# Kernel tuning notes

Measured on AMD Instinct MI355X. Metric: run time of the kernel, lower is better.

Reference implementation:

```python
import jax, jax.numpy as jnp
import numpy as np

H = 16
EPS = 1e-5

def _layernorm(x, gamma, beta):
    mu = jnp.mean(x, axis=-1, keepdims=True)
    var = jnp.var(x, axis=-1, keepdims=True)
    return (x - mu) * jax.lax.rsqrt(var + EPS) * gamma + beta

def setup_inputs() -> dict:
    key = jax.random.key(0)
    ks = jax.random.split(key, 5)
    B, T, E = 4, 2048, 1024
    D = E // H
    return {
        "x": jax.random.normal(ks[0], (B, T, E), dtype=jnp.float32),
        "Wqkv": jax.random.normal(ks[1], (E, 3 * E), dtype=jnp.float32) * (E ** -0.5),
        "bqkv": jax.random.normal(ks[2], (3 * E,), dtype=jnp.float32) * 0.02,
        "q_gamma": jnp.ones((D,), jnp.float32),
        "q_beta": jnp.zeros((D,), jnp.float32),
        "k_gamma": jnp.ones((D,), jnp.float32),
        "k_beta": jnp.zeros((D,), jnp.float32),
        "Wproj": jax.random.normal(ks[3], (E, E), dtype=jnp.float32) * (E ** -0.5),
        "bproj": jnp.zeros((E,), jnp.float32),
    }

def reference(x, Wqkv, bqkv, q_gamma, q_beta, k_gamma, k_beta, Wproj, bproj):
    B, T, E = x.shape
    D = E // H
    qkv = x @ Wqkv + bqkv                      # [B,T,3E]
    q, k, v = jnp.split(qkv, 3, axis=-1)
    # b t (h d) -> b h t d
    to_heads = lambda a: a.reshape(B, T, H, D).transpose(0, 2, 1, 3)
    q, k, v = to_heads(q), to_heads(k), to_heads(v)
    q = _layernorm(q, q_gamma, q_beta)
    k = _layernorm(k, k_gamma, k_beta)
    scale = 1.0 / jnp.sqrt(jnp.float32(D))
    scores = jnp.einsum('bhtd,bhsd->bhts', q, k) * scale   # [B,H,T,T]
    attn = jax.nn.softmax(scores, axis=-1)
    y = jnp.einsum('bhts,bhsd->bhtd', attn, v)             # [B,H,T,D]
    y = y.transpose(0, 2, 1, 3).reshape(B, T, E)           # b h t d -> b t (h d)
    return y @ Wproj + bproj
```

## Files before the change

### kernel.cpp

```cpp
#include <hip/hip_runtime.h>

#define Hn  16
#define Dh  64
#define Bb  4
#define Tn  2048
#define En  1024
#define Mn  8192
#define N1  3072
#define Kn  1024
#define BHT (Bb*Hn*Tn)

typedef __attribute__((ext_vector_type(8)))  short  short8;
typedef __attribute__((ext_vector_type(4)))  short  short4v;
typedef __attribute__((ext_vector_type(4)))  float  f32x4;
typedef __attribute__((ext_vector_type(8)))  __bf16 bf16x8;

__device__ __forceinline__ float b2f(short s) {
  unsigned u = ((unsigned)(unsigned short)s) << 16;
  return __builtin_bit_cast(float, u);
}
__device__ __forceinline__ short f2b(float f) {
  unsigned u = __builtin_bit_cast(unsigned, f);
  u += 0x7fffu + ((u >> 16) & 1u);
  return (short)(u >> 16);
}
__device__ __forceinline__ f32x4 mfma16(short8 a, short8 b, f32x4 c) {
  return __builtin_amdgcn_mfma_f32_16x16x32_bf16(
      __builtin_bit_cast(bf16x8, a), __builtin_bit_cast(bf16x8, b), c, 0, 0, 0);
}
__device__ __forceinline__ void gload16(const void* g, void* l) {
  __builtin_amdgcn_global_load_lds(
      (const __attribute__((address_space(1))) unsigned int*)g,
      (__attribute__((address_space(3))) unsigned int*)l, 16, 0, 0);
}

__global__ __launch_bounds__(256) void cvt_x_kernel(const float* __restrict__ x,
                                                    short* __restrict__ xb) {
  const size_t i = ((size_t)blockIdx.x * 256 + threadIdx.x) * 8;
  f32x4 a = *(const f32x4*)&x[i];
  f32x4 b = *(const f32x4*)&x[i + 4];
  short8 o;
  o[0]=f2b(a[0]); o[1]=f2b(a[1]); o[2]=f2b(a[2]); o[3]=f2b(a[3]);
  o[4]=f2b(b[0]); o[5]=f2b(b[1]); o[6]=f2b(b[2]); o[7]=f2b(b[3]);
  *(short8*)&xb[i] = o;
}

__global__ __launch_bounds__(256) void transpose_w_kernel(const float* __restrict__ in,
                                                          short* __restrict__ out,
                                                          int R, int C) {
  __shared__ float tile[32][33];
  const int tid = threadIdx.x;
  const int c0 = blockIdx.x * 32, r0 = blockIdx.y * 32;
  const int lr = tid >> 3, lc = (tid & 7) * 4;
  f32x4 v = *(const f32x4*)&in[(size_t)(r0 + lr) * C + c0 + lc];
  tile[lr][lc] = v[0]; tile[lr][lc+1] = v[1]; tile[lr][lc+2] = v[2]; tile[lr][lc+3] = v[3];
  __syncthreads();
  const int oc = tid >> 3, orr = (tid & 7) * 4;
  short4v ov;
  ov[0] = f2b(tile[orr][oc]);   ov[1] = f2b(tile[orr+1][oc]);
  ov[2] = f2b(tile[orr+2][oc]); ov[3] = f2b(tile[orr+3][oc]);
  *(short4v*)&out[(size_t)(c0 + oc) * R + r0 + orr] = ov;
}

template<int MODE>
__global__ __launch_bounds__(256) void gemm_kernel(
    const short* __restrict__ A, const short* __restrict__ Bt,
    const float* __restrict__ bias, float* __restrict__ Cf,
    short* __restrict__ qo, short* __restrict__ ko2, short* __restrict__ vo,
    int N, int NBX, int cpx) {
  __shared__ short As[4096];
  __shared__ short Bs[4096];
  const int lin = blockIdx.x;
  const int swz = (lin & 7) * cpx + (lin >> 3);
  const int bx = swz % NBX, by = swz / NBX;
  const int tid = threadIdx.x, lane = tid & 63, w = tid >> 6;
  const int rowBase = by * 128, colBase = bx * 128;
  f32x4 acc[4][4] = {};
  const int srow = tid >> 2, sk = (tid & 3) << 3;
  const short* Ag = A  + (size_t)(rowBase + srow) * Kn + sk;
  const short* Bg = Bt + (size_t)(colBase + srow) * Kn + sk;
  short* AsW = As + w * 512;
  short* BsW = Bs + w * 512;
  const int ar = (w >> 1) * 64, bc = (w & 1) * 64;
  const int lg8 = (lane >> 4) * 8, lr = lane & 15;

  for (int kt = 0; kt < Kn; kt += 32) {
    __syncthreads();
    gload16(Ag + kt,            AsW);
    gload16(Ag + kt + 64 * Kn,  AsW + 2048);
    gload16(Bg + kt,            BsW);
    gload16(Bg + kt + 64 * Kn,  BsW + 2048);
    __syncthreads();
    short8 af[4], bfr[4];
#pragma unroll
    for (int m = 0; m < 4; ++m) af[m]  = *(const short8*)&As[(ar + m*16 + lr)*32 + lg8];
#pragma unroll
    for (int n = 0; n < 4; ++n) bfr[n] = *(const short8*)&Bs[(bc + n*16 + lr)*32 + lg8];
#pragma unroll
    for (int m = 0; m < 4; ++m)
#pragma unroll
      for (int n = 0; n < 4; ++n)
        acc[m][n] = mfma16(af[m], bfr[n], acc[m][n]);
  }

  const int gr0 = rowBase + ar + (lane >> 4) * 4;
  const int gc0 = colBase + bc + lr;
#pragma unroll
  for (int m = 0; m < 4; ++m) {
#pragma unroll
    for (int n = 0; n < 4; ++n) {
      const int gc = gc0 + n * 16;
      const float bb = bias[gc];
#pragma unroll
      for (int r = 0; r < 4; ++r) {
        const int gr = gr0 + m * 16 + r;
        const float v = acc[m][n][r] + bb;
        if (MODE == 0) {
          Cf[(size_t)gr * N + gc] = v;
        } else {
          const int which = gc >> 10, e = gc & 1023;
          const int hh = e >> 6, d = e & 63;
          const int bidx = gr >> 11, t = gr & 2047;
          const size_t idx = ((size_t)(bidx * Hn + hh) * Tn + t) * Dh + d;
          short* dst = (which == 0) ? qo : (which == 1) ? ko2 : vo;
          dst[idx] = f2b(v);
        }
      }
    }
  }
}

__global__ __launch_bounds__(256) void ln_qk_kernel(short* __restrict__ qp, short* __restrict__ kp,
                                                    const float* __restrict__ qg, const float* __restrict__ qb,
                                                    const float* __restrict__ kg, const float* __restrict__ kb) {
  const int lane = threadIdx.x & 63;
  const int rp = blockIdx.x * 4 + (threadIdx.x >> 6);
  const size_t base = (size_t)rp * 64 + lane;
  float xq = b2f(qp[base]);
  float xk = b2f(kp[base]);
  float sq = xq, sk = xk;
#pragma unroll
  for (int off = 1; off < 64; off <<= 1) { sq += __shfl_xor(sq, off); sk += __shfl_xor(sk, off); }
  const float muq = sq * (1.f/64), muk = sk * (1.f/64);
  const float dq = xq - muq, dk = xk - muk;
  float vq = dq * dq, vk = dk * dk;
#pragma unroll
  for (int off = 1; off < 64; off <<= 1) { vq += __shfl_xor(vq, off); vk += __shfl_xor(vk, off); }
  const float rq = rsqrtf(vq * (1.f/64) + 1e-5f);
  const float rk = rsqrtf(vk * (1.f/64) + 1e-5f);
  const float yq = (dq * rq * qg[lane] + qb[lane]) * (0.125f * 1.44269504088896f);
  const float yk =  dk * rk * kg[lane] + kb[lane];
  qp[base] = f2b(yq);
  kp[base] = f2b(yk);
}

__global__ __launch_bounds__(256) void transpose_v_kernel(const short* __restrict__ vp,
                                                          short* __restrict__ vt) {
  __shared__ short tile[64][72];
  const int tid = threadIdx.x;
  const int bh = blockIdx.y, jt = blockIdx.x;
  const short* src = vp + ((size_t)bh * Tn + jt * 64) * Dh;
#pragma unroll
  for (int i = 0; i < 4; ++i) {
    const int idx = i * 1024 + tid * 4;
    short4v v = *(const short4v*)&src[idx];
    const int r = idx >> 6, c = idx & 63;
    tile[r][c] = v[0]; tile[r][c+1] = v[1]; tile[r][c+2] = v[2]; tile[r][c+3] = v[3];
  }
  __syncthreads();
  short* dst = vt + (size_t)bh * Dh * Tn + jt * 64;
#pragma unroll
  for (int i = 0; i < 4; ++i) {
    const int idx = i * 1024 + tid * 4;
    const int d = idx >> 6, t0 = idx & 63;
    short4v v;
    v[0] = tile[t0][d]; v[1] = tile[t0+1][d]; v[2] = tile[t0+2][d]; v[3] = tile[t0+3][d];
    *(short4v*)&dst[(size_t)d * Tn + t0] = v;
  }
}

__global__ __launch_bounds__(256) void flash_kernel(
    const short* __restrict__ qp, const short* __restrict__ kp,
    const short* __restrict__ vt, short* __restrict__ y) {
  __shared__ short Ks[2][4096];
  __shared__ short Vs[2][4096];
  __shared__ short Ps[4096];
  const int tid = threadIdx.x, lane = tid & 63, w = tid >> 6;
  const int lr = lane & 15, lg = lane >> 4;

  const int j0 = blockIdx.x;
  const int xcd = j0 & 7, kk0 = j0 >> 3;
  const int bh = 8 * xcd + (kk0 & 7), qt = kk0 >> 3;

  const int qrow0 = qt * 128 + w * 32;
  const short* qbase = qp + ((size_t)bh * Tn + qrow0) * Dh;

  short8 aq[2][2];
#pragma unroll
  for (int m = 0; m < 2; ++m)
#pragma unroll
    for (int kk = 0; kk < 2; ++kk)
      aq[m][kk] = *(const short8*)&qbase[(m*16 + lr)*64 + kk*32 + lg*8];

  short8 ones;
#pragma unroll
  for (int i = 0; i < 8; ++i) ones[i] = (short)0x3F80;

  f32x4 o[2][4] = {};
  f32x4 lacc[2] = {};
  float mrow[2][4];
#pragma unroll
  for (int m = 0; m < 2; ++m)
#pragma unroll
    for (int r = 0; r < 4; ++r) mrow[m][r] = -3e38f;

  const int srow = tid >> 3;
  const int sc = (tid & 7) * 8;
  short* Pw = Ps + w * 1024;
  const short* kb = kp + (size_t)bh * Tn * Dh;
  const short* vb = vt + (size_t)bh * Dh * Tn;

#define STAGE(jt, bsel)                                                   \
  {                                                                       \
    _Pragma("unroll")                                                     \
    for (int i = 0; i < 2; ++i) {                                         \
      const int row = i * 32 + srow;                                      \
      const int scs = sc ^ ((row & 7) << 3);                              \
      gload16(kb + (size_t)((jt) * 64 + row) * Dh + scs,                  \
              &Ks[bsel][w * 512 + i * 2048]);                             \
      gload16(vb + (size_t)row * Tn + (jt) * 64 + scs,                    \
              &Vs[bsel][w * 512 + i * 2048]);                             \
    }                                                                     \
  }

#define PSW(q) ((((q) & 3) << 3) ^ (((q) & 4) << 2))

  STAGE(0, 0);
  __syncthreads();

  for (int j = 0; j < Tn / 64; ++j) {
    const int cur = j & 1;
    if (j + 1 < Tn / 64) STAGE(j + 1, cur ^ 1);

    short8 bk[4][2];
#pragma unroll
    for (int n = 0; n < 4; ++n)
#pragma unroll
      for (int kk = 0; kk < 2; ++kk) {
        const int row = n * 16 + lr;
        bk[n][kk] = *(const short8*)&Ks[cur][row*64 + ((kk*32 + lg*8) ^ ((row & 7) << 3))];
      }
    f32x4 s[2][4] = {};
    __builtin_amdgcn_s_setprio(1);
#pragma unroll
    for (int m = 0; m < 2; ++m)
#pragma unroll
      for (int n = 0; n < 4; ++n) {
        s[m][n] = mfma16(aq[m][0], bk[n][0], s[m][n]);
        s[m][n] = mfma16(aq[m][1], bk[n][1], s[m][n]);
      }
    __builtin_amdgcn_s_setprio(0);

    float pm[2][4];
#pragma unroll
    for (int m = 0; m < 2; ++m)
#pragma unroll
      for (int r = 0; r < 4; ++r)
        pm[m][r] = fmaxf(fmaxf(s[m][0][r], s[m][1][r]), fmaxf(s[m][2][r], s[m][3][r]));
    int ok = 1;
#pragma unroll
    for (int m = 0; m < 2; ++m)
#pragma unroll
      for (int r = 0; r < 4; ++r)
        ok &= (pm[m][r] <= mrow[m][r] + 11.0f) ? 1 : 0;
    if (!__all(ok)) {
      float tm[2][4];
#pragma unroll
      for (int m = 0; m < 2; ++m)
#pragma unroll
        for (int r = 0; r < 4; ++r) tm[m][r] = pm[m][r];
#pragma unroll
      for (int off = 1; off < 16; off <<= 1)
#pragma unroll
        for (int m = 0; m < 2; ++m)
#pragma unroll
          for (int r = 0; r < 4; ++r)
            tm[m][r] = fmaxf(tm[m][r], __shfl_xor(tm[m][r], off));
#pragma unroll
      for (int m = 0; m < 2; ++m)
#pragma unroll
        for (int r = 0; r < 4; ++r) {
          const float mn = fmaxf(mrow[m][r], tm[m][r]);
          const float corr = __builtin_amdgcn_exp2f(mrow[m][r] - mn);
          lacc[m][r] *= corr;
#pragma unroll
          for (int dn = 0; dn < 4; ++dn) o[m][dn][r] *= corr;
          mrow[m][r] = mn;
        }
    }

    short8 bv[4][2];
#pragma unroll
    for (int dn = 0; dn < 4; ++dn)
#pragma unroll
      for (int kk = 0; kk < 2; ++kk) {
        const int row = dn * 16 + lr;
        bv[dn][kk] = *(const short8*)&Vs[cur][row*64 + ((kk*32 + lg*8) ^ ((row & 7) << 3))];
      }

#pragma unroll
    for (int m = 0; m < 2; ++m)
#pragma unroll
      for (int n = 0; n < 2; ++n)
#pragma unroll
        for (int r = 0; r < 4; ++r) {
          const float p = __builtin_amdgcn_exp2f(s[m][n][r] - mrow[m][r]);
          const unsigned u = __builtin_bit_cast(unsigned, p);
          const int q = m*16 + lg*4 + r;
          Pw[q*32 + ((n*16 + lr) ^ PSW(q))] = (short)(u >> 16);
        }
    short8 pa0[2];
#pragma unroll
    for (int m = 0; m < 2; ++m) {
      const int q = m*16 + lr;
      pa0[m] = *(const short8*)&Pw[q*32 + ((lg*8) ^ PSW(q))];
    }
    __builtin_amdgcn_s_setprio(1);
#pragma unroll
    for (int m = 0; m < 2; ++m) {
      lacc[m] = mfma16(pa0[m], ones, lacc[m]);
#pragma unroll
      for (int dn = 0; dn < 4; ++dn)
        o[m][dn] = mfma16(pa0[m], bv[dn][0], o[m][dn]);
    }
    __builtin_amdgcn_s_setprio(0);

#pragma unroll
    for (int m = 0; m < 2; ++m)
#pragma unroll
      for (int n = 0; n < 2; ++n)
#pragma unroll
        for (int r = 0; r < 4; ++r) {
          const float p = __builtin_amdgcn_exp2f(s[m][2 + n][r] - mrow[m][r]);
          const unsigned u = __builtin_bit_cast(unsigned, p);
          const int q = m*16 + lg*4 + r;
          Pw[q*32 + ((n*16 + lr) ^ PSW(q))] = (short)(u >> 16);
        }
    short8 pa1[2];
#pragma unroll
    for (int m = 0; m < 2; ++m) {
      const int q = m*16 + lr;
      pa1[m] = *(const short8*)&Pw[q*32 + ((lg*8) ^ PSW(q))];
    }
    __builtin_amdgcn_s_setprio(1);
#pragma unroll
    for (int m = 0; m < 2; ++m) {
      lacc[m] = mfma16(pa1[m], ones, lacc[m]);
#pragma unroll
      for (int dn = 0; dn < 4; ++dn)
        o[m][dn] = mfma16(pa1[m], bv[dn][1], o[m][dn]);
    }
    __builtin_amdgcn_s_setprio(0);

    __syncthreads();
  }
#undef STAGE
#undef PSW

  const int b = bh >> 4, hh = bh & 15;
  short* yb = y + (size_t)b * Tn * En + hh * 64;
#pragma unroll
  for (int m = 0; m < 2; ++m)
#pragma unroll
    for (int r = 0; r < 4; ++r) {
      const float rl = 1.0f / lacc[m][r];
      const int t = qrow0 + m*16 + lg*4 + r;
#pragma unroll
      for (int dn = 0; dn < 4; ++dn) {
        const int d = dn*16 + lr;
        yb[(size_t)t * En + d] = f2b(o[m][dn][r] * rl);
      }
    }
}

extern "C" void kernel_launch(void* const* d_in, const int* in_sizes, int n_in,
                              void* d_out, int out_size, void* d_ws, size_t ws_size,
                              hipStream_t stream) {
  const float* x     = (const float*)d_in[0];
  const float* Wqkv  = (const float*)d_in[1];
  const float* bqkv  = (const float*)d_in[2];
  const float* qg    = (const float*)d_in[3];
  const float* qb    = (const float*)d_in[4];
  const float* kg    = (const float*)d_in[5];
  const float* kb    = (const float*)d_in[6];
  const float* Wproj = (const float*)d_in[7];
  const float* bproj = (const float*)d_in[8];
  float* out = (float*)d_out;

  char* p = (char*)d_ws;
  short* xb     = (short*)p; p += (size_t)Mn * Kn * 2;
  short* wqkvT  = (short*)p; p += (size_t)N1 * Kn * 2;
  short* wprojT = (short*)p; p += (size_t)En * Kn * 2;
  short* qp     = (short*)p; p += (size_t)Mn * Kn * 2;
  short* kp     = (short*)p; p += (size_t)Mn * Kn * 2;
  short* vp     = (short*)p; p += (size_t)Mn * Kn * 2;
  short* vtb    = (short*)p; p += (size_t)Mn * Kn * 2;
  short* yb     = (short*)p; p += (size_t)Mn * Kn * 2;

  cvt_x_kernel<<<Mn * Kn / (256 * 8), 256, 0, stream>>>(x, xb);
  transpose_w_kernel<<<dim3(N1 / 32, Kn / 32), 256, 0, stream>>>(Wqkv, wqkvT, Kn, N1);
  transpose_w_kernel<<<dim3(En / 32, Kn / 32), 256, 0, stream>>>(Wproj, wprojT, Kn, En);
  gemm_kernel<1><<<(N1 / 128) * (Mn / 128), 256, 0, stream>>>(
      xb, wqkvT, bqkv, nullptr, qp, kp, vp, N1, N1 / 128, (N1 / 128) * (Mn / 128) / 8);
  ln_qk_kernel<<<BHT / 4, 256, 0, stream>>>(qp, kp, qg, qb, kg, kb);
  transpose_v_kernel<<<dim3(Tn / 64, Bb * Hn), 256, 0, stream>>>(vp, vtb);
  flash_kernel<<<1024, 256, 0, stream>>>(qp, kp, vtb, yb);
  gemm_kernel<0><<<(En / 128) * (Mn / 128), 256, 0, stream>>>(
      yb, wprojT, bproj, out, nullptr, nullptr, nullptr, En, En / 128, (En / 128) * (Mn / 128) / 8);
}
```

Baseline: 285.9 us.

## Fuse per-head Q/K layernorm and V transpose into QKV GEMM epilogue

Computes the per-head layernorm for Q and K directly in the QKV GEMM epilogue. Each 64-column warp tile is exactly one head, so the reduction uses shuffles across 16 lanes. V is written straight into the transposed [bh][d][t] layout, so the separate ln_qk and transpose_v kernels are removed along with their extra global round trips and launches. The risks are single-pass variance (E[x^2]-mu^2) with its lower numerical precision, and strided, uncoalesced V stores in the epilogue.

```diff
diff --git a/kernel.cpp b/kernel.cpp
--- a/kernel.cpp
+++ b/kernel.cpp
@@ -67,6 +67,8 @@
     const short* __restrict__ A, const short* __restrict__ Bt,
     const float* __restrict__ bias, float* __restrict__ Cf,
     short* __restrict__ qo, short* __restrict__ ko2, short* __restrict__ vo,
+    const float* __restrict__ qg, const float* __restrict__ qb,
+    const float* __restrict__ kg, const float* __restrict__ kb,
     int N, int NBX, int cpx) {
   __shared__ short As[4096];
   __shared__ short Bs[4096];
@@ -105,77 +107,76 @@
 
   const int gr0 = rowBase + ar + (lane >> 4) * 4;
   const int gc0 = colBase + bc + lr;
+
+  float bb[4];
+#pragma unroll
+  for (int n = 0; n < 4; ++n) bb[n] = bias[gc0 + n * 16];
+#pragma unroll
+  for (int m = 0; m < 4; ++m)
+#pragma unroll
+    for (int n = 0; n < 4; ++n)
+#pragma unroll
+      for (int r = 0; r < 4; ++r) acc[m][n][r] += bb[n];
+
+  if (MODE == 1) {
+    const int which = colBase >> 10;
+    if (which < 2) {
+      const float* gp = (which == 0) ? qg : kg;
+      const float* bp = (which == 0) ? qb : kb;
+      const float sc = (which == 0) ? 0.1803368801111204f : 1.0f;
+      float gam[4], bet[4];
+#pragma unroll
+      for (int n = 0; n < 4; ++n) { gam[n] = gp[n * 16 + lr]; bet[n] = bp[n * 16 + lr]; }
+#pragma unroll
+      for (int m = 0; m < 4; ++m)
+#pragma unroll
+        for (int r = 0; r < 4; ++r) {
+          float s1 = 0.f, s2 = 0.f;
+#pragma unroll
+          for (int n = 0; n < 4; ++n) {
+            const float v = acc[m][n][r];
+            s1 += v; s2 += v * v;
+          }
+#pragma unroll
+          for (int off = 1; off < 16; off <<= 1) {
+            s1 += __shfl_xor(s1, off);
+            s2 += __shfl_xor(s2, off);
+          }
+          const float mu = s1 * 0.015625f;
+          const float rs = rsqrtf(s2 * 0.015625f - mu * mu + 1e-5f);
+#pragma unroll
+          for (int n = 0; n < 4; ++n)
+            acc[m][n][r] = ((acc[m][n][r] - mu) * rs * gam[n] + bet[n]) * sc;
+        }
+    }
+  }
+
 #pragma unroll
   for (int m = 0; m < 4; ++m) {
 #pragma unroll
     for (int n = 0; n < 4; ++n) {
       const int gc = gc0 + n * 16;
-      const float bb = bias[gc];
 #pragma unroll
       for (int r = 0; r < 4; ++r) {
         const int gr = gr0 + m * 16 + r;
-        const float v = acc[m][n][r] + bb;
+        const float v = acc[m][n][r];
         if (MODE == 0) {
           Cf[(size_t)gr * N + gc] = v;
         } else {
           const int which = gc >> 10, e = gc & 1023;
           const int hh = e >> 6, d = e & 63;
           const int bidx = gr >> 11, t = gr & 2047;
-          const size_t idx = ((size_t)(bidx * Hn + hh) * Tn + t) * Dh + d;
-          short* dst = (which == 0) ? qo : (which == 1) ? ko2 : vo;
-          dst[idx] = f2b(v);
+          const int bh = bidx * Hn + hh;
+          if (which == 0) {
+            qo[((size_t)bh * Tn + t) * Dh + d] = f2b(v);
+          } else if (which == 1) {
+            ko2[((size_t)bh * Tn + t) * Dh + d] = f2b(v);
+          } else {
+            vo[((size_t)bh * Dh + d) * Tn + t] = f2b(v);
+          }
         }
       }
     }
-  }
-}
-
-__global__ __launch_bounds__(256) void ln_qk_kernel(short* __restrict__ qp, short* __restrict__ kp,
-                                                    const float* __restrict__ qg, const float* __restrict__ qb,
-                                                    const float* __restrict__ kg, const float* __restrict__ kb) {
-  const int lane = threadIdx.x & 63;
-  const int rp = blockIdx.x * 4 + (threadIdx.x >> 6);
-  const size_t base = (size_t)rp * 64 + lane;
-  float xq = b2f(qp[base]);
-  float xk = b2f(kp[base]);
-  float sq = xq, sk = xk;
-#pragma unroll
-  for (int off = 1; off < 64; off <<= 1) { sq += __shfl_xor(sq, off); sk += __shfl_xor(sk, off); }
-  const float muq = sq * (1.f/64), muk = sk * (1.f/64);
-  const float dq = xq - muq, dk = xk - muk;
-  float vq = dq * dq, vk = dk * dk;
-#pragma unroll
-  for (int off = 1; off < 64; off <<= 1) { vq += __shfl_xor(vq, off); vk += __shfl_xor(vk, off); }
-  const float rq = rsqrtf(vq * (1.f/64) + 1e-5f);
-  const float rk = rsqrtf(vk * (1.f/64) + 1e-5f);
-  const float yq = (dq * rq * qg[lane] + qb[lane]) * (0.125f * 1.44269504088896f);
-  const float yk =  dk * rk * kg[lane] + kb[lane];
-  qp[base] = f2b(yq);
-  kp[base] = f2b(yk);
-}
-
-__global__ __launch_bounds__(256) void transpose_v_kernel(const short* __restrict__ vp,
-                                                          short* __restrict__ vt) {
-  __shared__ short tile[64][72];
-  const int tid = threadIdx.x;
-  const int bh = blockIdx.y, jt = blockIdx.x;
-  const short* src = vp + ((size_t)bh * Tn + jt * 64) * Dh;
-#pragma unroll
-  for (int i = 0; i < 4; ++i) {
-    const int idx = i * 1024 + tid * 4;
-    short4v v = *(const short4v*)&src[idx];
-    const int r = idx >> 6, c = idx & 63;
-    tile[r][c] = v[0]; tile[r][c+1] = v[1]; tile[r][c+2] = v[2]; tile[r][c+3] = v[3];
-  }
-  __syncthreads();
-  short* dst = vt + (size_t)bh * Dh * Tn + jt * 64;
-#pragma unroll
-  for (int i = 0; i < 4; ++i) {
-    const int idx = i * 1024 + tid * 4;
-    const int d = idx >> 6, t0 = idx & 63;
-    short4v v;
-    v[0] = tile[t0][d]; v[1] = tile[t0+1][d]; v[2] = tile[t0+2][d]; v[3] = tile[t0+3][d];
-    *(short4v*)&dst[(size_t)d * Tn + t0] = v;
   }
 }
 
@@ -403,7 +404,6 @@
   short* wprojT = (short*)p; p += (size_t)En * Kn * 2;
   short* qp     = (short*)p; p += (size_t)Mn * Kn * 2;
   short* kp     = (short*)p; p += (size_t)Mn * Kn * 2;
-  short* vp     = (short*)p; p += (size_t)Mn * Kn * 2;
   short* vtb    = (short*)p; p += (size_t)Mn * Kn * 2;
   short* yb     = (short*)p; p += (size_t)Mn * Kn * 2;
 
@@ -411,10 +411,10 @@
   transpose_w_kernel<<<dim3(N1 / 32, Kn / 32), 256, 0, stream>>>(Wqkv, wqkvT, Kn, N1);
   transpose_w_kernel<<<dim3(En / 32, Kn / 32), 256, 0, stream>>>(Wproj, wprojT, Kn, En);
   gemm_kernel<1><<<(N1 / 128) * (Mn / 128), 256, 0, stream>>>(
-      xb, wqkvT, bqkv, nullptr, qp, kp, vp, N1, N1 / 128, (N1 / 128) * (Mn / 128) / 8);
-  ln_qk_kernel<<<BHT / 4, 256, 0, stream>>>(qp, kp, qg, qb, kg, kb);
-  transpose_v_kernel<<<dim3(Tn / 64, Bb * Hn), 256, 0, stream>>>(vp, vtb);
+      xb, wqkvT, bqkv, nullptr, qp, kp, vtb, qg, qb, kg, kb,
+      N1, N1 / 128, (N1 / 128) * (Mn / 128) / 8);
   flash_kernel<<<1024, 256, 0, stream>>>(qp, kp, vtb, yb);
   gemm_kernel<0><<<(En / 128) * (Mn / 128), 256, 0, stream>>>(
-      yb, wprojT, bproj, out, nullptr, nullptr, nullptr, En, En / 128, (En / 128) * (Mn / 128) / 8);
-}
+      yb, wprojT, bproj, out, nullptr, nullptr, nullptr, nullptr, nullptr, nullptr, nullptr,
+      En, En / 128, (En / 128) * (Mn / 128) / 8);
+}
```

Result: faster. 264.5 us (-7.5%).
